# Performance work log

Hardware: AMD Instinct MI355X
Metric: run time of the kernel (lower is better)

Reference implementation:

```python
import jax, jax.numpy as jnp
import numpy as np

DT = 0.05

def _conv(x, w):
    # x: [N,C,H,W], w: [O,I,kh,kw], SAME padding
    return jax.lax.conv_general_dilated(x, w, (1, 1), 'SAME',
                                        dimension_numbers=('NCHW', 'OIHW', 'NCHW'))

def _gru(h, x, wx, wh):
    # convolutional GRU cell (used for Bayesian jumps and SpatialGRU)
    xr, xz, xg = jnp.split(_conv(x, wx), 3, axis=1)
    hr, hz, hg = jnp.split(_conv(h, wh), 3, axis=1)
    r = jax.nn.sigmoid(xr + hr)
    z = jax.nn.sigmoid(xz + hz)
    g = jnp.tanh(xg + r * hg)
    return (1.0 - z) * h + z * g

def _ode_step(h, wrz, wg, dt):
    # GRU-ODE cell, explicit Euler: dh/dt = (1-z)*(g-h)
    r, z = jnp.split(jax.nn.sigmoid(_conv(h, wrz)), 2, axis=1)
    g = jnp.tanh(_conv(r * h, wg))
    return h + dt * (1.0 - z) * (g - h)

def _sgru(x, h0, wx, wh):
    # SpatialGRU: conv-GRU recurrence over the sequence dim
    def step(h, xt):
        h = _gru(h, xt, wx, wh)
        return h, h
    _, hs = jax.lax.scan(step, h0, x.transpose(1, 0, 2, 3, 4))
    return hs.transpose(1, 0, 2, 3, 4)

def setup_inputs() -> dict:
    key = jax.random.key(0)
    B, C, H, W = 2, 64, 64, 64
    Nc, Nl, NF = 3, 5, 6
    ks = jax.random.split(key, 16)
    f = lambda i, s: jax.random.normal(ks[i], s, jnp.float32)
    w = lambda i, s: 0.05 * jax.random.normal(ks[i], s, jnp.float32)
    inp = {}
    inp['future_prediction_input'] = f(0, (B, C, H, W))
    inp['camera_states'] = f(1, (B, Nc, C, H, W))
    inp['lidar_states'] = f(2, (B, Nl, C, H, W))
    # ragged obs times as exact multiples of DT; targets after all obs
    inp['camera_timestamp'] = jnp.broadcast_to(jnp.array([0., 2., 4.]) * DT, (B, Nc)).astype(jnp.float32)
    inp['lidar_timestamp'] = jnp.broadcast_to(jnp.array([1., 3., 5., 6., 7.]) * DT, (B, Nl)).astype(jnp.float32)
    inp['target_timestamp'] = jnp.broadcast_to(jnp.arange(8., 14.) * DT, (B, NF)).astype(jnp.float32)
    inp['ode_wrz'] = w(3, (2 * C, C, 3, 3))
    inp['ode_wg'] = w(4, (C, C, 3, 3))
    inp['jmp_wx'] = w(5, (3 * C, C, 3, 3))
    inp['jmp_wh'] = w(6, (3 * C, C, 3, 3))
    inp['sg0_wx'] = w(7, (3 * C, C, 3, 3))
    inp['sg0_wh'] = w(8, (3 * C, C, 3, 3))
    inp['sg1_wx'] = w(9, (3 * C, C, 3, 3))
    inp['sg1_wh'] = w(10, (3 * C, C, 3, 3))
    inp['res0_w1'] = w(11, (C, C, 3, 3))
    inp['res0_w2'] = w(12, (C, C, 3, 3))
    inp['dl_w1'] = w(13, (128, C, 3, 3))
    inp['dl_w2'] = w(14, (C, 128, 1, 1))
    return inp

def reference(future_prediction_input, camera_states, lidar_states,
              camera_timestamp, lidar_timestamp, target_timestamp,
              ode_wrz, ode_wg, jmp_wx, jmp_wh,
              sg0_wx, sg0_wh, sg1_wx, sg1_wh,
              res0_w1, res0_w2, dl_w1, dl_w2):
    dt = DT
    B, C, H, W = future_prediction_input.shape
    Nc, Nl, NF = camera_timestamp.shape[1], lidar_timestamp.shape[1], target_timestamp.shape[1]
    n_steps = Nc + Nl + NF  # static Euler grid covering all obs + target times
    # --- batched ragged merge: scatter obs onto the time grid (replaces per-sample dict sort) ---
    all_t = jnp.concatenate([camera_timestamp, lidar_timestamp], axis=1)          # [B, Nc+Nl]
    all_obs = jnp.concatenate([camera_states, lidar_states], axis=1)              # [B, Nc+Nl, C, H, W]
    steps = jnp.round(all_t / dt).astype(jnp.int32)
    bidx = jnp.arange(B)[:, None]
    grid = jnp.zeros((B, n_steps, C, H, W), all_obs.dtype).at[bidx, steps].set(all_obs)
    mask = jnp.zeros((B, n_steps), jnp.float32).at[bidx, steps].set(1.0)
    # --- ODE-RNN with Bayesian jumps: jump at obs, Euler-evolve between ---
    def ode_scan(h, xs):
        obs_t, m = xs
        hj = _gru(h, obs_t, jmp_wx, jmp_wh)
        h = jnp.where(m[:, None, None, None] > 0, hj, h)
        h = _ode_step(h, ode_wrz, ode_wg, dt)
        return h, h
    _, hs = jax.lax.scan(ode_scan, future_prediction_input,
                         (grid.transpose(1, 0, 2, 3, 4), mask.T))
    tsteps = jnp.round(target_timestamp / dt).astype(jnp.int32) - 1               # state after step k is time (k+1)*dt
    x = hs.transpose(1, 0, 2, 3, 4)[bidx, tsteps]                                 # [B, NF, C, H, W]
    auxilary_loss = jnp.float32(0.0)
    # --- spatial GRU stack + res blocks / DeepLab head ---
    hidden = x[:, 0]
    x = _sgru(x, hidden, sg0_wx, sg0_wh)
    xf = x.reshape(B * NF, C, H, W)
    xf = xf + _conv(jax.nn.relu(_conv(xf, res0_w1)), res0_w2)                     # residual Block
    x = xf.reshape(B, NF, C, H, W)
    x = _sgru(x, hidden, sg1_wx, sg1_wh)
    xf = x.reshape(B * NF, C, H, W)
    xf = _conv(jax.nn.relu(_conv(xf, dl_w1)), dl_w2)                              # DeepLabHead (3x3 -> relu -> 1x1)
    x = xf.reshape(B, NF, C, H, W)
    return (x, auxilary_loss)
```

## Files before the change

kernel.cpp:

```cpp
#include <hip/hip_runtime.h>
#include <stdint.h>

#define HWP 4096
#define SB  262144LL
#define FB  1572864LL
#define SLABU 1572864LL
#define DTC 0.05f

typedef short short4v __attribute__((ext_vector_type(4)));
typedef short short8v __attribute__((ext_vector_type(8)));
typedef float f32x16  __attribute__((ext_vector_type(16)));

__device__ __forceinline__ float sigm(float x) { return 1.f / (1.f + __expf(-x)); }
__device__ __forceinline__ float tanhf_(float x) {
  float a = fabsf(x);
  float t = __expf(-2.f * a);
  float r = (1.f - t) / (1.f + t);
  return x < 0.f ? -r : r;
}
__device__ __forceinline__ float gru1(float h, float xr, float hr, float xz,
                                      float hz, float xg, float hg) {
  float r = sigm(xr + hr);
  float z = sigm(xz + hz);
  float g = tanhf_(xg + r * hg);
  return (1.f - z) * h + z * g;
}
__device__ __forceinline__ float b2f(unsigned int u) {
  return __uint_as_float(u << 16);
}
__device__ __forceinline__ unsigned short f2b(float f) {
  unsigned int x = __float_as_uint(f);
  unsigned int r = (x + 0x7fffu + ((x >> 16) & 1u)) >> 16;
  return (unsigned short)r;
}

struct WJobs {
  const float* src[11];
  unsigned short* dst[11];
  int oc[11];
  int blk_off[12];
};

__global__ __launch_bounds__(256) void convert_all(WJobs jobs)
{
  int b = blockIdx.x;
  int j = 0;
  while (b >= jobs.blk_off[j + 1]) ++j;
  int g = (b - jobs.blk_off[j]) * 256 + threadIdx.x;
  if (g >= jobs.oc[j] * 64) return;
  const float* w = jobs.src[j];
  unsigned short* dst = jobs.dst[j];
  int oc = g >> 6, ic = g & 63;
  int ocg = oc >> 5, m = oc & 31;
  int kh = ic >> 4, ks = (ic >> 3) & 1, jj = ic & 7;
  int lane = m + 32 * ks;
#pragma unroll
  for (int t = 0; t < 9; ++t) {
    float v = w[(size_t)(oc * 64 + ic) * 9 + t];
    unsigned short hi = f2b(v);
    unsigned short lo = f2b(v - b2f(hi));
    size_t fb = ((size_t)(ocg * 4 + kh) * 9 + t) * 1024;
    dst[fb + (size_t)lane * 8 + jj] = hi;
    dst[fb + 512 + (size_t)lane * 8 + jj] = lo;
  }
}

template<int NR>
__device__ __forceinline__ void stage_rows(
    unsigned short (*lds)[2][66][68], int slot0,
    const float* __restrict__ in_img, int gy0, int tid)
{
  int px = tid & 63, icq = tid >> 6;
  int ic0 = icq * 16;
  float v[NR][16];
#pragma unroll
  for (int r = 0; r < NR; ++r) {
    int gy = gy0 + r;
    if (gy >= 0 && gy < 64) {
#pragma unroll
      for (int i = 0; i < 16; ++i)
        v[r][i] = in_img[(size_t)(ic0 + i) * HWP + (size_t)gy * 64 + px];
    } else {
#pragma unroll
      for (int i = 0; i < 16; ++i) v[r][i] = 0.f;
    }
  }
#pragma unroll
  for (int r = 0; r < NR; ++r) {
    unsigned short hi[16], lo[16];
#pragma unroll
    for (int i = 0; i < 16; ++i) {
      hi[i] = f2b(v[r][i]);
      lo[i] = f2b(v[r][i] - b2f(hi[i]));
    }
    unsigned short* dhi = &lds[slot0 + r][0][px + 1][ic0];
    unsigned short* dlo = &lds[slot0 + r][1][px + 1][ic0];
#pragma unroll
    for (int q = 0; q < 4; ++q) {
      uint2 ph, pl;
      ph.x = (unsigned)hi[q*4+0] | ((unsigned)hi[q*4+1] << 16);
      ph.y = (unsigned)hi[q*4+2] | ((unsigned)hi[q*4+3] << 16);
      pl.x = (unsigned)lo[q*4+0] | ((unsigned)lo[q*4+1] << 16);
      pl.y = (unsigned)lo[q*4+2] | ((unsigned)lo[q*4+3] << 16);
      *(uint2*)&dhi[q*4] = ph;
      *(uint2*)&dlo[q*4] = pl;
    }
  }
}

#define LOAD_B_SLOT(SLOT, kx)                                                 \
  {                                                                           \
    const unsigned short* bph = &lds[SLOT][0][x0 + n + kx][khb];              \
    const unsigned short* bpl = &lds[SLOT][1][x0 + n + kx][khb];              \
    bhi.lo = *(const short4v*)bph; bhi.hi = *(const short4v*)(bph + 4);       \
    blo.lo = *(const short4v*)bpl; blo.hi = *(const short4v*)(bpl + 4);       \
  }

#define MFMA3(CACC, AHI, ALO)                                                 \
  CACC = __builtin_amdgcn_mfma_f32_32x32x16_bf16(AHI, bhi, CACC, 0, 0, 0);    \
  CACC = __builtin_amdgcn_mfma_f32_32x32x16_bf16(ALO, bhi, CACC, 0, 0, 0);    \
  CACC = __builtin_amdgcn_mfma_f32_32x32x16_bf16(AHI, blo, CACC, 0, 0, 0);

__global__ __launch_bounds__(256) void gru_mfma(
    const float* __restrict__ hprev, long long h_is,
    const unsigned short* __restrict__ wfrag,
    const unsigned short* __restrict__ xcs,
    float* __restrict__ hout, long long o_is)
{
  __shared__ __align__(16) unsigned short lds[3][2][66][68];
  int bid = blockIdx.x;
  int img = bid >> 6, y = bid & 63;
  int tid = threadIdx.x;
  int wv = tid >> 6, lane = tid & 63;
  int wchg = wv >> 1, wpx = wv & 1;
  int x0 = wpx * 32;
  int n = lane & 31, ksub = lane >> 5;

  const float* in_img = hprev + (size_t)img * h_is;
  for (int i = tid; i < 3366; i += 256)
    ((uint4*)lds)[i] = make_uint4(0u, 0u, 0u, 0u);
  __syncthreads();
  stage_rows<3>(lds, 0, in_img, y - 1, tid);
  __syncthreads();

  f32x16 cr, cz, cg;
#pragma unroll
  for (int i = 0; i < 16; ++i) { cr[i] = 0.f; cz[i] = 0.f; cg[i] = 0.f; }

#pragma unroll
  for (int kh = 0; kh < 4; ++kh) {
    int khb = kh * 16 + ksub * 8;
#pragma unroll
    for (int kidx = 0; kidx < 9; ++kidx) {
      int ky = kidx / 3, kx = kidx - ky * 3;
      short8v bhi, blo;
      LOAD_B_SLOT(ky, kx);
      const unsigned short* apr =
          wfrag + (((size_t)wchg * 4 + kh) * 9 + kidx) * 1024 + (size_t)lane * 8;
      const unsigned short* apz = apr + (size_t)2 * 4 * 9 * 1024;
      const unsigned short* apg = apr + (size_t)4 * 4 * 9 * 1024;
      short8v arh = *(const short8v*)apr;
      short8v arl = *(const short8v*)(apr + 512);
      short8v azh = *(const short8v*)apz;
      short8v azl = *(const short8v*)(apz + 512);
      short8v agh = *(const short8v*)apg;
      short8v agl = *(const short8v*)(apg + 512);
      MFMA3(cr, arh, arl);
      MFMA3(cz, azh, azl);
      MFMA3(cg, agh, agl);
    }
  }

  const unsigned short* xcb = xcs + (size_t)img * 786432;
#pragma unroll
  for (int reg = 0; reg < 16; ++reg) {
    int crow = (reg & 3) + 8 * (reg >> 2) + 4 * ksub;
    int c = wchg * 32 + crow;
    size_t px = (size_t)y * 64 + x0 + n;
    float xr = b2f(xcb[(size_t)c * HWP + px]);
    float xz = b2f(xcb[(size_t)(c + 64) * HWP + px]);
    float xg = b2f(xcb[(size_t)(c + 128) * HWP + px]);
    float hv = b2f(lds[1][0][x0 + n + 1][c]) + b2f(lds[1][1][x0 + n + 1][c]);
    hout[(size_t)img * o_is + (size_t)c * HWP + px] =
        gru1(hv, xr, cr[reg], xz, cz[reg], xg, cg[reg]);
  }
}

__global__ __launch_bounds__(256) void rzodeg_mfma(
    const float* __restrict__ hsrc,
    const unsigned short* __restrict__ wrzf,
    const unsigned short* __restrict__ wgf,
    float* __restrict__ hdst,
    float* __restrict__ fr, float* __restrict__ hid)
{
  __shared__ __align__(16) unsigned short lds[5][2][66][68];
  int bid = blockIdx.x;
  int img = bid >> 6, y = bid & 63;
  int tid = threadIdx.x;
  int wv = tid >> 6, lane = tid & 63;
  int wchg = wv >> 1, wpx = wv & 1;
  int x0 = wpx * 32;
  int n = lane & 31, ksub = lane >> 5;

  for (int i = tid; i < 5 * 4 * 16; i += 256) {
    int row = i >> 4, q = i & 15;
    int slot = row >> 2, rem = row & 3;
    int plane = rem >> 1;
    int col = (rem & 1) ? 65 : 0;
    ((uint2*)&lds[slot][plane][col][0])[q] = make_uint2(0u, 0u);
  }
  const float* in_img = hsrc + (size_t)img * SB;
  stage_rows<5>(lds, 0, in_img, y - 2, tid);
  __syncthreads();

  f32x16 cr0, cr1, cr2, cz;
#pragma unroll
  for (int i = 0; i < 16; ++i) { cr0[i]=0.f; cr1[i]=0.f; cr2[i]=0.f; cz[i]=0.f; }

#pragma unroll
  for (int kh = 0; kh < 4; ++kh) {
    int khb = kh * 16 + ksub * 8;
#pragma unroll
    for (int kidx = 0; kidx < 9; ++kidx) {
      int ky = kidx / 3, kx = kidx - ky * 3;
      const unsigned short* apr =
          wrzf + (((size_t)wchg * 4 + kh) * 9 + kidx) * 1024 + (size_t)lane * 8;
      const unsigned short* apz = apr + (size_t)2 * 4 * 9 * 1024;
      short8v arh = *(const short8v*)apr;
      short8v arl = *(const short8v*)(apr + 512);
      short8v azh = *(const short8v*)apz;
      short8v azl = *(const short8v*)(apz + 512);
      { short8v bhi, blo; LOAD_B_SLOT(ky, kx);     MFMA3(cr0, arh, arl); }
      { short8v bhi, blo; LOAD_B_SLOT(ky + 1, kx); MFMA3(cr1, arh, arl);
                                                   MFMA3(cz,  azh, azl); }
      { short8v bhi, blo; LOAD_B_SLOT(ky + 2, kx); MFMA3(cr2, arh, arl); }
    }
  }

  float rv0[16], rv1[16], rv2[16], hk[16];
  {
    int pc = x0 + n + 1;
#pragma unroll
    for (int reg = 0; reg < 16; ++reg) {
      int crow = (reg & 3) + 8 * (reg >> 2) + 4 * ksub;
      int c = wchg * 32 + crow;
      float h0 = b2f(lds[1][0][pc][c]) + b2f(lds[1][1][pc][c]);
      float h1 = b2f(lds[2][0][pc][c]) + b2f(lds[2][1][pc][c]);
      float h2 = b2f(lds[3][0][pc][c]) + b2f(lds[3][1][pc][c]);
      rv0[reg] = sigm(cr0[reg]) * h0;
      rv1[reg] = sigm(cr1[reg]) * h1;
      rv2[reg] = sigm(cr2[reg]) * h2;
      hk[reg] = h1;
    }
  }
  __syncthreads();

  {
    int pc = x0 + n + 1;
#pragma unroll
    for (int reg = 0; reg < 16; ++reg) {
      int crow = (reg & 3) + 8 * (reg >> 2) + 4 * ksub;
      int c = wchg * 32 + crow;
      unsigned short h0 = f2b(rv0[reg]), l0 = f2b(rv0[reg] - b2f(h0));
      unsigned short h1 = f2b(rv1[reg]), l1 = f2b(rv1[reg] - b2f(h1));
      unsigned short h2 = f2b(rv2[reg]), l2 = f2b(rv2[reg] - b2f(h2));
      lds[0][0][pc][c] = h0; lds[0][1][pc][c] = l0;
      lds[1][0][pc][c] = h1; lds[1][1][pc][c] = l1;
      lds[2][0][pc][c] = h2; lds[2][1][pc][c] = l2;
    }
  }
  __syncthreads();

  f32x16 cg;
#pragma unroll
  for (int i = 0; i < 16; ++i) cg[i] = 0.f;
#pragma unroll
  for (int kh = 0; kh < 4; ++kh) {
    int khb = kh * 16 + ksub * 8;
#pragma unroll
    for (int kidx = 0; kidx < 9; ++kidx) {
      int ky = kidx / 3, kx = kidx - ky * 3;
      const unsigned short* ap =
          wgf + (((size_t)wchg * 4 + kh) * 9 + kidx) * 1024 + (size_t)lane * 8;
      short8v ahi = *(const short8v*)ap;
      short8v alo = *(const short8v*)(ap + 512);
      short8v bhi, blo;
      LOAD_B_SLOT(ky, kx);
      MFMA3(cg, ahi, alo);
    }
  }

#pragma unroll
  for (int reg = 0; reg < 16; ++reg) {
    int crow = (reg & 3) + 8 * (reg >> 2) + 4 * ksub;
    int c = wchg * 32 + crow;
    size_t pxo = (size_t)y * 64 + x0 + n;
    size_t idx = (size_t)img * SB + (size_t)c * HWP + pxo;
    float z = sigm(cz[reg]);
    float h = hk[reg];
    float o = h + DTC * (1.f - z) * (tanhf_(cg[reg]) - h);
    hdst[idx] = o;
    if (fr)  fr[(size_t)img * FB + (size_t)c * HWP + pxo] = o;
    if (hid) hid[idx] = o;
  }
}

__global__ __launch_bounds__(256) void conv_mfma(
    const float* __restrict__ in_base, long long s1, long long s2,
    const float* __restrict__ cam, const float* __restrict__ lid, int s0,
    const unsigned short* __restrict__ wfrag, int OC,
    float* __restrict__ out_f32, unsigned short* __restrict__ out_b16,
    long long o1, long long o2, int flags)
{
  __shared__ __align__(16) unsigned short lds[4][2][66][68];

  int bpe = (OC >> 6) << 5;
  int bid = blockIdx.x;
  int e = bid / bpe; int r = bid - e * bpe;
  int ocb = r >> 5; int yb = r & 31;
  int y0 = yb << 1;
  int tid = threadIdx.x;
  int wv = tid >> 6, lane = tid & 63;
  int wocg = wv >> 1, wpx = wv & 1;
  int oc0w = ocb * 64 + wocg * 32;
  int x0 = wpx * 32;
  int n = lane & 31, ksub = lane >> 5;

  const float* in_img;
  if (cam) {
    int s = s0 + (e >> 1); int img = e & 1;
    int isLid = (0xEA >> s) & 1;
    int frm = isLid ? (s < 5 ? (s >> 1) : s - 3) : (s >> 1);
    in_img = isLid ? lid + ((size_t)img * 5 + frm) * SB
                   : cam + ((size_t)img * 3 + frm) * SB;
  } else {
    in_img = in_base + (size_t)(e >> 1) * s1 + (size_t)(e & 1) * s2;
  }
  size_t obase = (size_t)(e >> 1) * o1 + (size_t)(e & 1) * o2;

  for (int i = tid; i < 4488; i += 256)
    ((uint4*)lds)[i] = make_uint4(0u, 0u, 0u, 0u);
  __syncthreads();
  stage_rows<4>(lds, 0, in_img, y0 - 1, tid);
  __syncthreads();

  size_t wfbase = (size_t)(oc0w >> 5) * 4;

  f32x16 c0, c1;
#pragma unroll
  for (int i = 0; i < 16; ++i) { c0[i] = 0.f; c1[i] = 0.f; }

#pragma unroll
  for (int kh = 0; kh < 4; ++kh) {
    int khb = kh * 16 + ksub * 8;
#pragma unroll
    for (int kidx = 0; kidx < 9; ++kidx) {
      int ky = kidx / 3, kx = kidx - ky * 3;
      const unsigned short* ap =
          wfrag + ((wfbase + kh) * 9 + kidx) * 1024 + (size_t)lane * 8;
      short8v ahi = *(const short8v*)ap;
      short8v alo = *(const short8v*)(ap + 512);
      short8v bhi, blo;
      LOAD_B_SLOT(ky, kx);
      MFMA3(c0, ahi, alo);
      LOAD_B_SLOT(ky + 1, kx);
      MFMA3(c1, ahi, alo);
    }
  }

  auto epilogue = [&](const f32x16& c, int y) {
#pragma unroll
    for (int reg = 0; reg < 16; ++reg) {
      int row = (reg & 3) + 8 * (reg >> 2) + 4 * ksub;
      int oc = oc0w + row;
      float v = c[reg];
      if (flags & 1) v = fmaxf(v, 0.f);
      size_t off = obase + (size_t)oc * HWP + (size_t)y * 64 + (x0 + n);
      if (out_b16) {
        out_b16[off] = f2b(v);
      } else {
        if (flags & 2) v += out_f32[off];
        out_f32[off] = v;
      }
    }
  };
  epilogue(c0, y0);
  epilogue(c1, y0 + 1);
}

__global__ __launch_bounds__(256) void conv1x1_k(
    const unsigned short* __restrict__ in, const float* __restrict__ wt,
    float* __restrict__ out)
{
  int bid = blockIdx.x;
  int img = bid >> 5; int r = bid & 31; int pxb = r >> 3; int ocg = r & 7;
  int px = pxb * 1024 + threadIdx.x * 4;
  const unsigned short* ip = in + (size_t)img * 128 * HWP + px;
  float4 acc[8] = {};
  for (int ic = 0; ic < 128; ++ic) {
    ushort4 u = *(const ushort4*)&ip[(size_t)ic * HWP];
    float4 v;
    v.x = b2f(u.x); v.y = b2f(u.y); v.z = b2f(u.z); v.w = b2f(u.w);
#pragma unroll
    for (int j = 0; j < 8; ++j) {
      float w = wt[(ocg * 8 + j) * 128 + ic];
      acc[j].x += v.x * w; acc[j].y += v.y * w;
      acc[j].z += v.z * w; acc[j].w += v.w * w;
    }
  }
#pragma unroll
  for (int j = 0; j < 8; ++j) {
    int oc = ocg * 8 + j;
    float* dst = out + ((size_t)img * 64 + oc) * HWP + px;
    *(float4*)dst = acc[j];
  }
}

__global__ __launch_bounds__(256) void copy_k(
    const float* __restrict__ in, float* __restrict__ out)
{
  int i = blockIdx.x * 256 + threadIdx.x;
  ((float4*)out)[i] = ((const float4*)in)[i];
}

__global__ void aux_k(float* out) { out[0] = 0.f; }

extern "C" void kernel_launch(void* const* d_in, const int* in_sizes, int n_in,
                              void* d_out, int out_size, void* d_ws, size_t ws_size,
                              hipStream_t stream)
{
  const float* fpi = (const float*)d_in[0];
  const float* cam = (const float*)d_in[1];
  const float* lid = (const float*)d_in[2];
  const float* w_ode_rz = (const float*)d_in[6];
  const float* w_ode_g  = (const float*)d_in[7];
  const float* w_jmp_x  = (const float*)d_in[8];
  const float* w_jmp_h  = (const float*)d_in[9];
  const float* w_sg0_x  = (const float*)d_in[10];
  const float* w_sg0_h  = (const float*)d_in[11];
  const float* w_sg1_x  = (const float*)d_in[12];
  const float* w_sg1_h  = (const float*)d_in[13];
  const float* w_res_1  = (const float*)d_in[14];
  const float* w_res_2  = (const float*)d_in[15];
  const float* w_dl_1   = (const float*)d_in[16];
  const float* w_dl_2   = (const float*)d_in[17];

  float* ws     = (float*)d_ws;
  float* frames = ws;
  float* hidden = ws + 3145728;
  float* h_a    = ws + 3670016;
  float* h_b    = ws + 4194304;
  unsigned short* xcu    = (unsigned short*)(ws + 5505024);
  unsigned short* wbuf   = (unsigned short*)(ws + 7864320);
  float* big_res = ws + 3670016;
  unsigned short* big_dl = (unsigned short*)(ws + 3670016);

  unsigned short* wjx  = wbuf;
  unsigned short* ws0x = wbuf + 221184;
  unsigned short* ws1x = wbuf + 442368;
  unsigned short* wre1 = wbuf + 663552;
  unsigned short* wre2 = wbuf + 737280;
  unsigned short* wdl1 = wbuf + 811008;
  unsigned short* wjh  = wbuf + 958464;
  unsigned short* ws0h = wbuf + 1179648;
  unsigned short* ws1h = wbuf + 1400832;
  unsigned short* wrz  = wbuf + 1622016;
  unsigned short* wg   = wbuf + 1769472;

  WJobs jobs;
  const float* srcs[11] = {w_jmp_x, w_sg0_x, w_sg1_x, w_jmp_h, w_sg0_h, w_sg1_h,
                           w_dl_1, w_ode_rz, w_res_1, w_res_2, w_ode_g};
  unsigned short* dsts[11] = {wjx, ws0x, ws1x, wjh, ws0h, ws1h,
                              wdl1, wrz, wre1, wre2, wg};
  int ocs[11] = {192, 192, 192, 192, 192, 192, 128, 128, 64, 64, 64};
  int off = 0;
  for (int j = 0; j < 11; ++j) {
    jobs.src[j] = srcs[j]; jobs.dst[j] = dsts[j]; jobs.oc[j] = ocs[j];
    jobs.blk_off[j] = off; off += ocs[j] / 4;
  }
  jobs.blk_off[11] = off;
  convert_all<<<off, 256, 0, stream>>>(jobs);

  copy_k<<<512, 256, 0, stream>>>(fpi, h_a);

  const int batch_s0[3] = {0, 3, 6};
  const int batch_t1[3] = {3, 6, 13};
  float* cur = h_a;
  for (int b = 0; b < 3; ++b) {
    int nobs = (b < 2) ? 3 : 2;
    conv_mfma<<<nobs * 2 * 3 * 32, 256, 0, stream>>>(
        nullptr, 0, 0, cam, lid, batch_s0[b], wjx, 192,
        nullptr, xcu, SLABU, 786432, 0);
    for (int t = batch_s0[b]; t < batch_t1[b]; ++t) {
      float* fr  = (t >= 7) ? frames + (long long)(t - 7) * SB : nullptr;
      float* hid = (t == 7) ? hidden : nullptr;
      if (t < 8) {
        gru_mfma<<<128, 256, 0, stream>>>(
            h_a, SB, wjh, xcu + (long long)(t - batch_s0[b]) * SLABU, h_b, SB);
        rzodeg_mfma<<<128, 256, 0, stream>>>(h_b, wrz, wg, h_a, fr, hid);
        cur = h_a;
      } else {
        float* dst = (cur == h_a) ? h_b : h_a;
        rzodeg_mfma<<<128, 256, 0, stream>>>(cur, wrz, wg, dst, fr, nullptr);
        cur = dst;
      }
    }
  }

  for (int b = 0; b < 2; ++b) {
    conv_mfma<<<576, 256, 0, stream>>>(frames + (long long)(b * 3) * SB, SB, FB,
                                       nullptr, nullptr, 0, ws0x, 192,
                                       nullptr, xcu, SLABU, 786432, 0);
    for (int tl = 0; tl < 3; ++tl) {
      int f = b * 3 + tl;
      const float* hp = (f == 0) ? hidden : frames + (long long)(f - 1) * SB;
      long long hbs = (f == 0) ? SB : FB;
      gru_mfma<<<128, 256, 0, stream>>>(hp, hbs, ws0h,
                                        xcu + (long long)tl * SLABU,
                                        frames + (long long)f * SB, FB);
    }
  }

  conv_mfma<<<384, 256, 0, stream>>>(frames, 2 * SB, SB, nullptr, nullptr, 0,
                                     wre1, 64, big_res, nullptr, 2 * SB, SB, 1);
  conv_mfma<<<384, 256, 0, stream>>>(big_res, 2 * SB, SB, nullptr, nullptr, 0,
                                     wre2, 64, frames, nullptr, 2 * SB, SB, 2);

  for (int b = 0; b < 2; ++b) {
    conv_mfma<<<576, 256, 0, stream>>>(frames + (long long)(b * 3) * SB, SB, FB,
                                       nullptr, nullptr, 0, ws1x, 192,
                                       nullptr, xcu, SLABU, 786432, 0);
    for (int tl = 0; tl < 3; ++tl) {
      int f = b * 3 + tl;
      const float* hp = (f == 0) ? hidden : frames + (long long)(f - 1) * SB;
      long long hbs = (f == 0) ? SB : FB;
      gru_mfma<<<128, 256, 0, stream>>>(hp, hbs, ws1h,
                                        xcu + (long long)tl * SLABU,
                                        frames + (long long)f * SB, FB);
    }
  }

  conv_mfma<<<768, 256, 0, stream>>>(frames, 2 * SB, SB, nullptr, nullptr, 0,
                                     wdl1, 128, nullptr, big_dl,
                                     1048576, 524288, 1);
  conv1x1_k<<<384, 256, 0, stream>>>(big_dl, w_dl_2, (float*)d_out);

  aux_k<<<1, 1, 0, stream>>>((float*)d_out + 3145728);
}
```

Measured before the change: 1.108 ms.

## Fuse two SpatialGRU steps per kernel and move the 1x1 head conv to MFMA

Adds gru2_mfma, which computes one GRU step on three rows (with halo recompute) and keeps the new hidden state in LDS to run the next step inside the same kernel. This halves the number of recurrent launches and global round-trips for the SpatialGRU stacks. Input convolutions are batched over four frames at once into a larger slab. The scalar 1x1 DeepLab conv is replaced with a split-bf16 MFMA kernel using pre-converted weights. The cost is three times the recurrent conv work for the first step in each fused kernel, plus higher register pressure.

```diff
diff --git a/kernel.cpp b/kernel.cpp
--- a/kernel.cpp
+++ b/kernel.cpp
@@ -63,6 +63,23 @@
     dst[fb + (size_t)lane * 8 + jj] = hi;
     dst[fb + 512 + (size_t)lane * 8 + jj] = lo;
   }
+}
+
+__global__ __launch_bounds__(256) void convert_1x1(
+    const float* __restrict__ w, unsigned short* __restrict__ dst)
+{
+  int g = blockIdx.x * 256 + threadIdx.x;
+  if (g >= 64 * 128) return;
+  int oc = g >> 7, ic = g & 127;
+  int ocg = oc >> 5, m = oc & 31;
+  int k = ic >> 4, ksub = (ic >> 3) & 1, j = ic & 7;
+  int lane = m + 32 * ksub;
+  float v = w[(size_t)oc * 128 + ic];
+  unsigned short hi = f2b(v);
+  unsigned short lo = f2b(v - b2f(hi));
+  size_t fb = (size_t)(ocg * 8 + k) * 1024;
+  dst[fb + (size_t)lane * 8 + j] = hi;
+  dst[fb + 512 + (size_t)lane * 8 + j] = lo;
 }
 
 template<int NR>
@@ -186,6 +203,155 @@
   }
 }
 
+__global__ __launch_bounds__(256) void gru2_mfma(
+    const float* __restrict__ hprev, long long h_is,
+    const unsigned short* __restrict__ wfrag,
+    const unsigned short* __restrict__ xcs0,
+    const unsigned short* __restrict__ xcs1,
+    float* __restrict__ out0, float* __restrict__ out1)
+{
+  __shared__ __align__(16) unsigned short lds[5][2][66][68];
+  int bid = blockIdx.x;
+  int img = bid >> 6, y = bid & 63;
+  int tid = threadIdx.x;
+  int wv = tid >> 6, lane = tid & 63;
+  int wchg = wv >> 1, wpx = wv & 1;
+  int x0 = wpx * 32;
+  int n = lane & 31, ksub = lane >> 5;
+
+  for (int i = tid; i < 5 * 4 * 16; i += 256) {
+    int row = i >> 4, q = i & 15;
+    int slot = row >> 2, rem = row & 3;
+    int plane = rem >> 1;
+    int col = (rem & 1) ? 65 : 0;
+    ((uint2*)&lds[slot][plane][col][0])[q] = make_uint2(0u, 0u);
+  }
+  stage_rows<5>(lds, 0, hprev + (size_t)img * h_is, y - 2, tid);
+  __syncthreads();
+
+  f32x16 cR[3], cZ[3], cG[3];
+#pragma unroll
+  for (int j = 0; j < 3; ++j)
+#pragma unroll
+    for (int i = 0; i < 16; ++i) { cR[j][i] = 0.f; cZ[j][i] = 0.f; cG[j][i] = 0.f; }
+
+#pragma unroll
+  for (int kh = 0; kh < 4; ++kh) {
+    int khb = kh * 16 + ksub * 8;
+#pragma unroll
+    for (int kidx = 0; kidx < 9; ++kidx) {
+      int ky = kidx / 3, kx = kidx - ky * 3;
+      const unsigned short* apr =
+          wfrag + (((size_t)wchg * 4 + kh) * 9 + kidx) * 1024 + (size_t)lane * 8;
+      const unsigned short* apz = apr + (size_t)2 * 4 * 9 * 1024;
+      const unsigned short* apg = apr + (size_t)4 * 4 * 9 * 1024;
+      short8v arh = *(const short8v*)apr;
+      short8v arl = *(const short8v*)(apr + 512);
+      short8v azh = *(const short8v*)apz;
+      short8v azl = *(const short8v*)(apz + 512);
+      short8v agh = *(const short8v*)apg;
+      short8v agl = *(const short8v*)(apg + 512);
+#pragma unroll
+      for (int j = 0; j < 3; ++j) {
+        short8v bhi, blo;
+        LOAD_B_SLOT(j + ky, kx);
+        MFMA3(cR[j], arh, arl);
+        MFMA3(cZ[j], azh, azl);
+        MFMA3(cG[j], agh, agl);
+      }
+    }
+  }
+
+  float hnew[3][16];
+  const unsigned short* xcb0 = xcs0 + (size_t)img * 786432;
+  int pc = x0 + n + 1;
+#pragma unroll
+  for (int j = 0; j < 3; ++j) {
+    int ry = y - 1 + j;
+    bool valid = (ry >= 0 && ry < 64);
+#pragma unroll
+    for (int reg = 0; reg < 16; ++reg) {
+      int crow = (reg & 3) + 8 * (reg >> 2) + 4 * ksub;
+      int c = wchg * 32 + crow;
+      if (valid) {
+        size_t px = (size_t)ry * 64 + x0 + n;
+        float xr = b2f(xcb0[(size_t)c * HWP + px]);
+        float xz = b2f(xcb0[(size_t)(c + 64) * HWP + px]);
+        float xg = b2f(xcb0[(size_t)(c + 128) * HWP + px]);
+        float hold = b2f(lds[1 + j][0][pc][c]) + b2f(lds[1 + j][1][pc][c]);
+        hnew[j][reg] = gru1(hold, xr, cR[j][reg], xz, cZ[j][reg],
+                            xg, cG[j][reg]);
+      } else {
+        hnew[j][reg] = 0.f;
+      }
+    }
+  }
+
+#pragma unroll
+  for (int reg = 0; reg < 16; ++reg) {
+    int crow = (reg & 3) + 8 * (reg >> 2) + 4 * ksub;
+    int c = wchg * 32 + crow;
+    out0[(size_t)img * FB + (size_t)c * HWP + (size_t)y * 64 + x0 + n] =
+        hnew[1][reg];
+  }
+
+  __syncthreads();
+#pragma unroll
+  for (int j = 0; j < 3; ++j) {
+#pragma unroll
+    for (int reg = 0; reg < 16; ++reg) {
+      int crow = (reg & 3) + 8 * (reg >> 2) + 4 * ksub;
+      int c = wchg * 32 + crow;
+      unsigned short hi = f2b(hnew[j][reg]);
+      unsigned short lo = f2b(hnew[j][reg] - b2f(hi));
+      lds[j][0][pc][c] = hi;
+      lds[j][1][pc][c] = lo;
+    }
+  }
+  __syncthreads();
+
+  f32x16 cr, cz, cg;
+#pragma unroll
+  for (int i = 0; i < 16; ++i) { cr[i] = 0.f; cz[i] = 0.f; cg[i] = 0.f; }
+
+#pragma unroll
+  for (int kh = 0; kh < 4; ++kh) {
+    int khb = kh * 16 + ksub * 8;
+#pragma unroll
+    for (int kidx = 0; kidx < 9; ++kidx) {
+      int ky = kidx / 3, kx = kidx - ky * 3;
+      short8v bhi, blo;
+      LOAD_B_SLOT(ky, kx);
+      const unsigned short* apr =
+          wfrag + (((size_t)wchg * 4 + kh) * 9 + kidx) * 1024 + (size_t)lane * 8;
+      const unsigned short* apz = apr + (size_t)2 * 4 * 9 * 1024;
+      const unsigned short* apg = apr + (size_t)4 * 4 * 9 * 1024;
+      short8v arh = *(const short8v*)apr;
+      short8v arl = *(const short8v*)(apr + 512);
+      short8v azh = *(const short8v*)apz;
+      short8v azl = *(const short8v*)(apz + 512);
+      short8v agh = *(const short8v*)apg;
+      short8v agl = *(const short8v*)(apg + 512);
+      MFMA3(cr, arh, arl);
+      MFMA3(cz, azh, azl);
+      MFMA3(cg, agh, agl);
+    }
+  }
+
+  const unsigned short* xcb1 = xcs1 + (size_t)img * 786432;
+#pragma unroll
+  for (int reg = 0; reg < 16; ++reg) {
+    int crow = (reg & 3) + 8 * (reg >> 2) + 4 * ksub;
+    int c = wchg * 32 + crow;
+    size_t px = (size_t)y * 64 + x0 + n;
+    float xr = b2f(xcb1[(size_t)c * HWP + px]);
+    float xz = b2f(xcb1[(size_t)(c + 64) * HWP + px]);
+    float xg = b2f(xcb1[(size_t)(c + 128) * HWP + px]);
+    out1[(size_t)img * FB + (size_t)c * HWP + px] =
+        gru1(hnew[1][reg], xr, cr[reg], xz, cz[reg], xg, cg[reg]);
+  }
+}
+
 __global__ __launch_bounds__(256) void rzodeg_mfma(
     const float* __restrict__ hsrc,
     const unsigned short* __restrict__ wrzf,
@@ -388,31 +554,55 @@
   epilogue(c1, y0 + 1);
 }
 
-__global__ __launch_bounds__(256) void conv1x1_k(
-    const unsigned short* __restrict__ in, const float* __restrict__ wt,
+__global__ __launch_bounds__(256) void conv1x1_mfma(
+    const unsigned short* __restrict__ in,
+    const unsigned short* __restrict__ wfrag,
     float* __restrict__ out)
 {
+  __shared__ unsigned short lds1[64][132];
   int bid = blockIdx.x;
-  int img = bid >> 5; int r = bid & 31; int pxb = r >> 3; int ocg = r & 7;
-  int px = pxb * 1024 + threadIdx.x * 4;
-  const unsigned short* ip = in + (size_t)img * 128 * HWP + px;
-  float4 acc[8] = {};
-  for (int ic = 0; ic < 128; ++ic) {
-    ushort4 u = *(const ushort4*)&ip[(size_t)ic * HWP];
-    float4 v;
-    v.x = b2f(u.x); v.y = b2f(u.y); v.z = b2f(u.z); v.w = b2f(u.w);
-#pragma unroll
-    for (int j = 0; j < 8; ++j) {
-      float w = wt[(ocg * 8 + j) * 128 + ic];
-      acc[j].x += v.x * w; acc[j].y += v.y * w;
-      acc[j].z += v.z * w; acc[j].w += v.w * w;
-    }
-  }
-#pragma unroll
-  for (int j = 0; j < 8; ++j) {
-    int oc = ocg * 8 + j;
-    float* dst = out + ((size_t)img * 64 + oc) * HWP + px;
-    *(float4*)dst = acc[j];
+  int img = bid >> 6; int pt = bid & 63;
+  int px0 = pt * 64;
+  int tid = threadIdx.x;
+  int wv = tid >> 6, lane = tid & 63;
+  int wocg = wv >> 1, wpx = wv & 1;
+  int x0 = wpx * 32;
+  int n = lane & 31, ksub = lane >> 5;
+
+  const unsigned short* ip = in + (size_t)img * 128 * HWP + px0;
+  {
+    int px = tid & 63, icq = tid >> 6;
+#pragma unroll
+    for (int i = 0; i < 32; ++i) {
+      int ic = icq * 32 + i;
+      lds1[px][ic] = ip[(size_t)ic * HWP + px];
+    }
+  }
+  __syncthreads();
+
+  f32x16 c;
+#pragma unroll
+  for (int i = 0; i < 16; ++i) c[i] = 0.f;
+
+#pragma unroll
+  for (int k = 0; k < 8; ++k) {
+    const unsigned short* ap =
+        wfrag + (size_t)(wocg * 8 + k) * 1024 + (size_t)lane * 8;
+    short8v ahi = *(const short8v*)ap;
+    short8v alo = *(const short8v*)(ap + 512);
+    int khb = k * 16 + ksub * 8;
+    const unsigned short* bp = &lds1[x0 + n][khb];
+    short8v b;
+    b.lo = *(const short4v*)bp; b.hi = *(const short4v*)(bp + 4);
+    c = __builtin_amdgcn_mfma_f32_32x32x16_bf16(ahi, b, c, 0, 0, 0);
+    c = __builtin_amdgcn_mfma_f32_32x32x16_bf16(alo, b, c, 0, 0, 0);
+  }
+
+#pragma unroll
+  for (int reg = 0; reg < 16; ++reg) {
+    int row = (reg & 3) + 8 * (reg >> 2) + 4 * ksub;
+    int oc = wocg * 32 + row;
+    out[((size_t)img * 64 + oc) * HWP + px0 + x0 + n] = c[reg];
   }
 }
 
@@ -450,10 +640,12 @@
   float* hidden = ws + 3145728;
   float* h_a    = ws + 3670016;
   float* h_b    = ws + 4194304;
-  unsigned short* xcu    = (unsigned short*)(ws + 5505024);
-  unsigned short* wbuf   = (unsigned short*)(ws + 7864320);
+  unsigned short* xcu  = (unsigned short*)(ws + 5505024);
+  unsigned short* xcu4 = (unsigned short*)(ws + 4718592);
+  unsigned short* wbuf = (unsigned short*)(ws + 7864320);
   float* big_res = ws + 3670016;
   unsigned short* big_dl = (unsigned short*)(ws + 3670016);
+  unsigned short* wdl2f  = (unsigned short*)(ws + 8785920);
 
   unsigned short* wjx  = wbuf;
   unsigned short* ws0x = wbuf + 221184;
@@ -480,6 +672,7 @@
   }
   jobs.blk_off[11] = off;
   convert_all<<<off, 256, 0, stream>>>(jobs);
+  convert_1x1<<<32, 256, 0, stream>>>(w_dl_2, wdl2f);
 
   copy_k<<<512, 256, 0, stream>>>(fpi, h_a);
 
@@ -507,43 +700,43 @@
     }
   }
 
-  for (int b = 0; b < 2; ++b) {
-    conv_mfma<<<576, 256, 0, stream>>>(frames + (long long)(b * 3) * SB, SB, FB,
-                                       nullptr, nullptr, 0, ws0x, 192,
-                                       nullptr, xcu, SLABU, 786432, 0);
-    for (int tl = 0; tl < 3; ++tl) {
-      int f = b * 3 + tl;
-      const float* hp = (f == 0) ? hidden : frames + (long long)(f - 1) * SB;
-      long long hbs = (f == 0) ? SB : FB;
-      gru_mfma<<<128, 256, 0, stream>>>(hp, hbs, ws0h,
-                                        xcu + (long long)tl * SLABU,
-                                        frames + (long long)f * SB, FB);
-    }
-  }
+  conv_mfma<<<768, 256, 0, stream>>>(frames, SB, FB, nullptr, nullptr, 0,
+                                     ws0x, 192, nullptr, xcu4, SLABU, 786432, 0);
+  gru2_mfma<<<128, 256, 0, stream>>>(hidden, SB, ws0h,
+                                     xcu4, xcu4 + SLABU,
+                                     frames, frames + SB);
+  gru2_mfma<<<128, 256, 0, stream>>>(frames + SB, FB, ws0h,
+                                     xcu4 + 2 * SLABU, xcu4 + 3 * SLABU,
+                                     frames + 2 * SB, frames + 3 * SB);
+  conv_mfma<<<384, 256, 0, stream>>>(frames + 4 * SB, SB, FB, nullptr, nullptr, 0,
+                                     ws0x, 192, nullptr, xcu4, SLABU, 786432, 0);
+  gru2_mfma<<<128, 256, 0, stream>>>(frames + 3 * SB, FB, ws0h,
+                                     xcu4, xcu4 + SLABU,
+                                     frames + 4 * SB, frames + 5 * SB);
 
   conv_mfma<<<384, 256, 0, stream>>>(frames, 2 * SB, SB, nullptr, nullptr, 0,
                                      wre1, 64, big_res, nullptr, 2 * SB, SB, 1);
   conv_mfma<<<384, 256, 0, stream>>>(big_res, 2 * SB, SB, nullptr, nullptr, 0,
                                      wre2, 64, frames, nullptr, 2 * SB, SB, 2);
 
-  for (int b = 0; b < 2; ++b) {
-    conv_mfma<<<576, 256, 0, stream>>>(frames + (long long)(b * 3) * SB, SB, FB,
-                                       nullptr, nullptr, 0, ws1x, 192,
-                                       nullptr, xcu, SLABU, 786432, 0);
-    for (int tl = 0; tl < 3; ++tl) {
-      int f = b * 3 + tl;
-      const float* hp = (f == 0) ? hidden : frames + (long long)(f - 1) * SB;
-      long long hbs = (f == 0) ? SB : FB;
-      gru_mfma<<<128, 256, 0, stream>>>(hp, hbs, ws1h,
-                                        xcu + (long long)tl * SLABU,
-                                        frames + (long long)f * SB, FB);
-    }
-  }
+  conv_mfma<<<768, 256, 0, stream>>>(frames, SB, FB, nullptr, nullptr, 0,
+                                     ws1x, 192, nullptr, xcu4, SLABU, 786432, 0);
+  gru2_mfma<<<128, 256, 0, stream>>>(hidden, SB, ws1h,
+                                     xcu4, xcu4 + SLABU,
+                                     frames, frames + SB);
+  gru2_mfma<<<128, 256, 0, stream>>>(frames + SB, FB, ws1h,
+                                     xcu4 + 2 * SLABU, xcu4 + 3 * SLABU,
+                                     frames + 2 * SB, frames + 3 * SB);
+  conv_mfma<<<384, 256, 0, stream>>>(frames + 4 * SB, SB, FB, nullptr, nullptr, 0,
+                                     ws1x, 192, nullptr, xcu4, SLABU, 786432, 0);
+  gru2_mfma<<<128, 256, 0, stream>>>(frames + 3 * SB, FB, ws1h,
+                                     xcu4, xcu4 + SLABU,
+                                     frames + 4 * SB, frames + 5 * SB);
 
   conv_mfma<<<768, 256, 0, stream>>>(frames, 2 * SB, SB, nullptr, nullptr, 0,
                                      wdl1, 128, nullptr, big_dl,
                                      1048576, 524288, 1);
-  conv1x1_k<<<384, 256, 0, stream>>>(big_dl, w_dl_2, (float*)d_out);
+  conv1x1_mfma<<<768, 256, 0, stream>>>(big_dl, wdl2f, (float*)d_out);
 
   aux_k<<<1, 1, 0, stream>>>((float*)d_out + 3145728);
 }
```

Result: slower. 1.338 ms (+20.7%).
